# Kernel tuning notes

Measured on AMD Instinct MI355X. Metric: run time of the kernel, lower is better.

The kernel has to match this reference:

```python
import jax, jax.numpy as jnp
import numpy as np

E = 2          # n_modalities
HQ = 16        # n_heads
HK = 8         # n_kv_heads
HD = 128       # head_dim
DIM = 2048
BS = 2
SEQ = 2048
EPS = 1e-6
ROPE_THETA = 10000.0


def _rmsnorm(x, w):
    # x: (..., d), w broadcastable to x
    return x * jax.lax.rsqrt(jnp.mean(x * x, axis=-1, keepdims=True) + EPS) * w


def _apply_rope(t, cos, sin):
    # t: (bs, seq, H, HD); cos/sin: (seq, HD//2). Complex rotation on pairs.
    t2 = t.reshape(*t.shape[:-1], HD // 2, 2)
    t0, t1 = t2[..., 0], t2[..., 1]
    c = cos[None, :, None, :]
    s = sin[None, :, None, :]
    out = jnp.stack([t0 * c - t1 * s, t0 * s + t1 * c], axis=-1)
    return out.reshape(t.shape)


def setup_inputs() -> dict:
    key = jax.random.key(0)
    ks = jax.random.split(key, 8)
    pos = jnp.arange(SEQ, dtype=jnp.float32)
    inv_freq = 1.0 / (ROPE_THETA ** (jnp.arange(0, HD, 2, dtype=jnp.float32) / HD))
    ang = pos[:, None] * inv_freq[None, :]  # (SEQ, HD//2)
    return {
        "x": jax.random.normal(ks[0], (BS, SEQ, DIM), jnp.float32),
        "freqs_cos": jnp.cos(ang),
        "freqs_sin": jnp.sin(ang),
        "wq": jax.random.normal(ks[1], (E, DIM, HQ * HD), jnp.float32) * 0.02,
        "wk": jax.random.normal(ks[2], (E, DIM, HK * HD), jnp.float32) * 0.02,
        "wv": jax.random.normal(ks[3], (E, DIM, HK * HD), jnp.float32) * 0.02,
        "wo": jax.random.normal(ks[4], (E, HQ * HD, DIM), jnp.float32) * 0.02,
        "q_norm_w": jnp.ones((E, HD), jnp.float32),
        "k_norm_w": jnp.ones((E, HD), jnp.float32),
        "attn_norm_w": jnp.ones((E, DIM), jnp.float32),
        "modality_ids": jax.random.randint(ks[5], (BS * SEQ,), 0, E, jnp.int32),
    }


def reference(x, freqs_cos, freqs_sin, wq, wk, wv, wo,
              q_norm_w, k_norm_w, attn_norm_w, modality_ids):
    bs, seq, dim = x.shape
    xf = x.reshape(-1, dim)  # (N, dim)
    onehot = (modality_ids[None, :] == jnp.arange(E, dtype=modality_ids.dtype)[:, None]).astype(x.dtype)  # (E, N)

    # Per-modality QKV projections + QK RMSNorm, then combine by modality id
    q = jnp.einsum('nd,edh->enh', xf, wq).reshape(E, -1, HQ, HD)
    q = _rmsnorm(q, q_norm_w[:, None, None, :])
    q = jnp.einsum('en,enhd->nhd', onehot, q).reshape(bs, seq, HQ, HD)

    k = jnp.einsum('nd,edh->enh', xf, wk).reshape(E, -1, HK, HD)
    k = _rmsnorm(k, k_norm_w[:, None, None, :])
    k = jnp.einsum('en,enhd->nhd', onehot, k).reshape(bs, seq, HK, HD)

    v = jnp.einsum('nd,edh->enh', xf, wv).reshape(E, -1, HK, HD)
    v = jnp.einsum('en,enhd->nhd', onehot, v).reshape(bs, seq, HK, HD)

    # RoPE
    q = _apply_rope(q, freqs_cos, freqs_sin)
    k = _apply_rope(k, freqs_cos, freqs_sin)

    # repeat_kv for GQA
    n_rep = HQ // HK
    k = jnp.repeat(k, n_rep, axis=2)
    v = jnp.repeat(v, n_rep, axis=2)

    # Global causal SDPA
    qh = jnp.swapaxes(q, 1, 2)  # (bs, HQ, seq, HD)
    kh = jnp.swapaxes(k, 1, 2)
    vh = jnp.swapaxes(v, 1, 2)
    scores = jnp.einsum('bhqd,bhkd->bhqk', qh, kh) / jnp.sqrt(jnp.asarray(HD, x.dtype))
    causal = jnp.tril(jnp.ones((seq, seq), dtype=bool))
    scores = jnp.where(causal[None, None], scores, jnp.asarray(-1e30, x.dtype))
    attn = jax.nn.softmax(scores, axis=-1)
    out = jnp.einsum('bhqk,bhkd->bhqd', attn, vh)
    out_flat = jnp.swapaxes(out, 1, 2).reshape(-1, HQ * HD)  # (N, HQ*HD)

    # Per-modality output projection + RMSNorm, combine
    o = jnp.einsum('nh,ehd->end', out_flat, wo)  # (E, N, dim)
    o = _rmsnorm(o, attn_norm_w[:, None, :])
    o = jnp.einsum('en,end->nd', onehot, o)
    return o.reshape(bs, seq, dim)
```

## Files before the change

### kernel.cpp

```cpp
#include <hip/hip_runtime.h>

#define E_ 2
#define HQ_ 16
#define HK_ 8
#define HD_ 128
#define DIM_ 2048
#define BS_ 2
#define SEQ_ 2048
#define NTOK 4096

typedef unsigned short ushort_t;
typedef short bf16x8 __attribute__((ext_vector_type(8)));
typedef unsigned short ushort8 __attribute__((ext_vector_type(8)));
typedef float f32x4 __attribute__((ext_vector_type(4)));

#define MFMA(a, b, c) __builtin_amdgcn_mfma_f32_16x16x32_bf16(a, b, c, 0, 0, 0)

__device__ __forceinline__ unsigned short f2bf(float f) {
  unsigned u = __builtin_bit_cast(unsigned, f);
  u = (u + 0x7FFFu + ((u >> 16) & 1u)) >> 16;
  return (unsigned short)u;
}
__device__ __forceinline__ float bf2f(unsigned short h) {
  unsigned u = ((unsigned)h) << 16;
  return __builtin_bit_cast(float, u);
}

__device__ __forceinline__ void glds16(const void* g, void* s) {
  __builtin_amdgcn_global_load_lds(
      (const __attribute__((address_space(1))) unsigned int*)g,
      (__attribute__((address_space(3))) unsigned int*)s, 16, 0, 0);
}

__global__ __launch_bounds__(1024) void build_crow(const int* __restrict__ ids,
                                                   int* __restrict__ cnt, int* __restrict__ crow) {
  __shared__ int sc[1024];
  __shared__ int total0;
  const int t = threadIdx.x;
  int id4[4];
  int c = 0;
  for (int j = 0; j < 4; j++) {
    id4[j] = ids[t * 4 + j];
    c += (id4[j] == 0);
  }
  sc[t] = c;
  __syncthreads();
  for (int off = 1; off < 1024; off <<= 1) {
    int v = sc[t];
    int add = (t >= off) ? sc[t - off] : 0;
    __syncthreads();
    sc[t] = v + add;
    __syncthreads();
  }
  if (t == 1023) total0 = sc[1023];
  __syncthreads();
  const int cnt0 = total0;
  if (t == 0) {
    cnt[0] = cnt0;
    cnt[1] = NTOK - cnt0;
  }
  int p0 = sc[t] - c;
  int r0 = 0;
  for (int j = 0; j < 4; j++) {
    int n = t * 4 + j;
    int cr;
    if (id4[j] == 0) {
      cr = p0 + r0;
      r0++;
    } else {
      cr = cnt0 + (n - (p0 + r0));
    }
    crow[n] = cr;
  }
}

__global__ __launch_bounds__(256) void convert_scatter(const float* __restrict__ x,
                                                       const int* __restrict__ crow,
                                                       ushort_t* __restrict__ xb) {
  const int token = blockIdx.x;
  const int cr = crow[token];
  const long src = (long)token * DIM_ + threadIdx.x * 8;
  const long dst = (long)cr * DIM_ + threadIdx.x * 8;
  float4 a = *(const float4*)(x + src);
  float4 b = *(const float4*)(x + src + 4);
  ushort8 o;
  o[0] = f2bf(a.x); o[1] = f2bf(a.y); o[2] = f2bf(a.z); o[3] = f2bf(a.w);
  o[4] = f2bf(b.x); o[5] = f2bf(b.y); o[6] = f2bf(b.z); o[7] = f2bf(b.w);
  *(ushort8*)(xb + dst) = o;
}

__global__ __launch_bounds__(256) void transpose_f2b(const float* __restrict__ in,
                                                     ushort_t* __restrict__ out, int K, int N,
                                                     long inE, long outE, int outBase) {
  __shared__ float tile[32][33];
  int e = blockIdx.z;
  const float* inp = in + (long)e * inE;
  ushort_t* outp = out + (long)e * outE;
  int n0 = blockIdx.x * 32, k0 = blockIdx.y * 32;
  int tx = threadIdx.x & 31, ty = threadIdx.x >> 5;
  for (int i = 0; i < 4; i++)
    tile[ty + i * 8][tx] = inp[(long)(k0 + ty + i * 8) * N + n0 + tx];
  __syncthreads();
  for (int i = 0; i < 4; i++)
    outp[(long)(outBase + n0 + ty + i * 8) * K + k0 + tx] = f2bf(tile[tx][ty + i * 8]);
}

__global__ __launch_bounds__(256) void transpose_v(const ushort_t* __restrict__ qkv,
                                                   const int* __restrict__ crow,
                                                   ushort_t* __restrict__ vt) {
  __shared__ ushort_t tile[32][34];
  int z = blockIdx.z;
  int b = z / HK_, hk = z % HK_;
  int s0 = blockIdx.x * 32, d0 = blockIdx.y * 32;
  int tx = threadIdx.x & 31, ty = threadIdx.x >> 5;
  for (int i = 0; i < 4; i++) {
    int cr = crow[b * SEQ_ + s0 + ty + i * 8];
    tile[ty + i * 8][tx] = qkv[(long)cr * 4096 + 3072 + hk * 128 + d0 + tx];
  }
  __syncthreads();
  for (int i = 0; i < 4; i++)
    vt[((long)(b * HK_ + hk) * 128 + d0 + ty + i * 8) * SEQ_ + s0 + tx] = tile[tx][ty + i * 8];
}

__global__ __launch_bounds__(512, 2) void gemm_bt_8ph(const ushort_t* __restrict__ A,
                                                      const ushort_t* __restrict__ BT,
                                                      ushort_t* __restrict__ C, int K, int Nc,
                                                      const int* __restrict__ cnt, long btE) {
  __shared__ __align__(16) char lds[131072];
  const int bm = blockIdx.x, bn = blockIdx.y, e = blockIdx.z;
  const int cnt0 = cnt[0];
  const int scnt = e ? (NTOK - cnt0) : cnt0;
  if (bm * 256 >= scnt) return;
  const int sbase = e ? cnt0 : 0;
  const ushort_t* Bte = BT + (long)e * btE;

  const int t = threadIdx.x, w = t >> 6, lane = t & 63;
  const int quad = lane >> 4, l16 = lane & 15;
  const int wr = w >> 2, wc = w & 3;
  const int nh = wc >> 1;

  const int arow0 = sbase + bm * 256;
  const int brow0 = bn * 256;

  const int srow = t >> 2;
  const int lc = ((t & 3) - (srow >> 1)) & 3;
  int ga0 = arow0 + srow;        if (ga0 > NTOK - 1) ga0 = NTOK - 1;
  int ga1 = arow0 + 128 + srow;  if (ga1 > NTOK - 1) ga1 = NTOK - 1;
  const ushort_t* sA0 = A + (long)ga0 * K + lc * 8;
  const ushort_t* sA1 = A + (long)ga1 * K + lc * 8;
  const ushort_t* sB0 = Bte + (long)(brow0 + srow) * K + lc * 8;
  const ushort_t* sB1 = Bte + (long)(brow0 + 128 + srow) * K + lc * 8;

  char* ldsw = (char*)lds + w * 1024;
  const int aoffF = wr * 16384;
  const int boffF = 32768 + nh * 16384;

  f32x4 acc[8][4];
#pragma unroll
  for (int i = 0; i < 8; i++)
#pragma unroll
    for (int j = 0; j < 4; j++) acc[i][j] = (f32x4){0.f, 0.f, 0.f, 0.f};

  bf16x8 bfr[4];

#define STAGE_A(bufbyte, ks, kk)                                              \
  glds16(sA0 + (kk) + (ks) * 32, ldsw + (bufbyte) + (0 * 2 + (ks)) * 8192);   \
  glds16(sA1 + (kk) + (ks) * 32, ldsw + (bufbyte) + (1 * 2 + (ks)) * 8192);
#define STAGE_B(bufbyte, ks, kk)                                                      \
  glds16(sB0 + (kk) + (ks) * 32, ldsw + (bufbyte) + 32768 + (0 * 2 + (ks)) * 8192);   \
  glds16(sB1 + (kk) + (ks) * 32, ldsw + (bufbyte) + 32768 + (1 * 2 + (ks)) * 8192);

#define PHASE(ks, mfh, LOADB, STG)                                                        \
  {                                                                                       \
    bf16x8 af[4];                                                                         \
    _Pragma("unroll") for (int i = 0; i < 4; i++) {                                       \
      const int r = ((mfh)*4 + i) * 16 + l16;                                             \
      af[i] = *(const bf16x8*)(Ab + (ks)*8192 + r * 64 + ((quad + (r >> 1)) & 3) * 16);   \
    }                                                                                     \
    if (LOADB) {                                                                          \
      _Pragma("unroll") for (int nf = 0; nf < 4; nf++) {                                  \
        const int r = (wc & 1) * 64 + nf * 16 + l16;                                      \
        bfr[nf] = *(const bf16x8*)(Bb + (ks)*8192 + r * 64 + ((quad + (r >> 1)) & 3) * 16); \
      }                                                                                   \
    }                                                                                     \
    STG;                                                                                  \
    __builtin_amdgcn_s_barrier();                                                         \
    asm volatile("s_waitcnt lgkmcnt(0)" ::: "memory");                                    \
    __builtin_amdgcn_sched_barrier(0);                                                    \
    __builtin_amdgcn_s_setprio(1);                                                        \
    _Pragma("unroll") for (int i = 0; i < 4; i++)                                         \
        _Pragma("unroll") for (int nf = 0; nf < 4; nf++)                                  \
            acc[(mfh)*4 + i][nf] = MFMA(af[i], bfr[nf], acc[(mfh)*4 + i][nf]);            \
    __builtin_amdgcn_s_setprio(0);                                                        \
    __builtin_amdgcn_s_barrier();                                                         \
  }

  STAGE_A(0, 0, 0);
  STAGE_B(0, 0, 0);
  STAGE_A(0, 1, 0);
  STAGE_B(0, 1, 0);
  asm volatile("s_waitcnt vmcnt(0)" ::: "memory");
  __builtin_amdgcn_s_barrier();

  const int NT = K >> 6;
  for (int kt = 0; kt < NT; kt++) {
    const int bufb = (kt & 1) << 16;
    const int nxtb = bufb ^ 65536;
    const int k1 = (kt + 1) << 6;
    const bool st = (kt + 1) < NT;
    const char* Ab = (const char*)lds + bufb + aoffF;
    const char* Bb = (const char*)lds + bufb + boffF;

    PHASE(0, 0, 1,
          if (st) { STAGE_A(nxtb, 0, k1); asm volatile("s_waitcnt vmcnt(4)" ::: "memory"); }
          else { asm volatile("s_waitcnt vmcnt(0)" ::: "memory"); })
    PHASE(0, 1, 0,
          if (st) { STAGE_B(nxtb, 0, k1); asm volatile("s_waitcnt vmcnt(4)" ::: "memory"); }
          else { asm volatile("s_waitcnt vmcnt(0)" ::: "memory"); })
    PHASE(1, 0, 1,
          if (st) { STAGE_A(nxtb, 1, k1); asm volatile("s_waitcnt vmcnt(4)" ::: "memory"); }
          else { asm volatile("s_waitcnt vmcnt(0)" ::: "memory"); })
    PHASE(1, 1, 0,
          if (st) { STAGE_B(nxtb, 1, k1); asm volatile("s_waitcnt vmcnt(4)" ::: "memory"); }
          else { asm volatile("s_waitcnt vmcnt(0)" ::: "memory"); })
  }
#undef PHASE
#undef STAGE_A
#undef STAGE_B

#pragma unroll
  for (int mf = 0; mf < 8; mf++) {
#pragma unroll
    for (int reg = 0; reg < 4; reg++) {
      const int rl = wr * 128 + mf * 16 + quad * 4 + reg;
      if (bm * 256 + rl >= scnt) continue;
      ushort_t* Cp = C + (long)(arow0 + rl) * Nc + brow0 + wc * 64 + l16;
#pragma unroll
      for (int nf = 0; nf < 4; nf++) Cp[nf * 16] = f2bf(acc[mf][nf][reg]);
    }
  }
}

__global__ __launch_bounds__(256) void fuse_rmsrope(
    const ushort_t* __restrict__ qkv, const int* __restrict__ crow, const float* __restrict__ qw,
    const float* __restrict__ kw, const float* __restrict__ fc, const float* __restrict__ fs,
    const int* __restrict__ ids, ushort_t* __restrict__ qout, ushort_t* __restrict__ kout) {
  const int token = blockIdx.x;
  const int slot = blockIdx.y * 4 + (threadIdx.x >> 6);
  const int lane = threadIdx.x & 63;
  const int b = token >> 11, s = token & 2047;
  const int e = ids[token];
  const int cr = crow[token];
  const bool isq = slot < 16;
  const int h = isq ? slot : slot - 16;
  const ushort_t* src = qkv + (long)cr * 4096 + (isq ? slot * 128 : 2048 + h * 128);
  unsigned pv = *(const unsigned*)(src + 2 * lane);
  float v0 = bf2f((unsigned short)pv), v1 = bf2f((unsigned short)(pv >> 16));
  float ss = v0 * v0 + v1 * v1;
  ss += __shfl_xor(ss, 32); ss += __shfl_xor(ss, 16); ss += __shfl_xor(ss, 8);
  ss += __shfl_xor(ss, 4);  ss += __shfl_xor(ss, 2);  ss += __shfl_xor(ss, 1);
  float r = rsqrtf(ss * (1.0f / 128.0f) + 1e-6f);
  const float* nw = (isq ? qw : kw) + e * 128;
  v0 *= r * nw[2 * lane];
  v1 *= r * nw[2 * lane + 1];
  float c = fc[s * 64 + lane], sn = fs[s * 64 + lane];
  float o0 = v0 * c - v1 * sn;
  float o1 = v0 * sn + v1 * c;
  ushort_t* dst;
  if (isq) {
    const float QS = 0.08838834764831845f * 1.4426950408889634f;
    o0 *= QS; o1 *= QS;
    dst = qout + ((long)(b * HQ_ + h) * SEQ_ + s) * 128;
  } else {
    dst = kout + ((long)(b * HK_ + h) * SEQ_ + s) * 128;
  }
  *(unsigned*)(dst + 2 * lane) = (unsigned)f2bf(o0) | ((unsigned)f2bf(o1) << 16);
}

__global__ __launch_bounds__(256, 2) void attn_kernel(const ushort_t* __restrict__ Q,
                                                      const ushort_t* __restrict__ K,
                                                      const ushort_t* __restrict__ VT,
                                                      const int* __restrict__ crow,
                                                      ushort_t* __restrict__ O) {
  __shared__ __align__(16) ushort_t Qs[64 * 128];
  __shared__ __align__(16) ushort_t Ks[64 * 128];
  __shared__ __align__(16) ushort_t Vs[128 * 64];
  __shared__ __align__(16) ushort_t Ps[4][16][72];

  const int bh = blockIdx.y;
  const int b = bh >> 4, h = bh & 15, hk = h >> 1;
  const int qi = 31 - blockIdx.x;
  const int q0 = qi * 64;
  const int t = threadIdx.x, w = t >> 6, lane = t & 63;
  const int quad = lane >> 4, l16 = lane & 15;

  const ushort_t* qbase = Q + ((long)(b * HQ_ + h) * SEQ_) * HD_;
  const ushort_t* kbase = K + ((long)(b * HK_ + hk) * SEQ_) * HD_;
  const ushort_t* vtbase = VT + ((long)(b * HK_ + hk) * HD_) * SEQ_;

  for (int c = 0; c < 4; c++) {
    int lin = c * 4096 + w * 1024 + lane * 16;
    int row = lin >> 8;
    int gc = (((lin >> 4) & 15) - row) & 15;
    glds16(qbase + (long)(q0 + row) * HD_ + gc * 8, (char*)Qs + c * 4096 + w * 1024);
  }
  __syncthreads();
  bf16x8 qf[4];
  {
    int row = w * 16 + l16;
    for (int kk = 0; kk < 4; kk++) {
      int cl = (kk * 4 + quad + row) & 15;
      qf[kk] = *(const bf16x8*)((const char*)Qs + row * 256 + cl * 16);
    }
  }

  const f32x4 zero = {0.f, 0.f, 0.f, 0.f};
  f32x4 oa[8];
  for (int i = 0; i < 8; i++) oa[i] = zero;
  float rs[4] = {0.f, 0.f, 0.f, 0.f};

  const int nkt = qi + 1;
  for (int kt = 0; kt < nkt; kt++) {
    const int s0 = kt * 64;
    for (int c = 0; c < 4; c++) {
      int lin = c * 4096 + w * 1024 + lane * 16;
      int row = lin >> 8;
      int gc = (((lin >> 4) & 15) - row) & 15;
      glds16(kbase + (long)(s0 + row) * HD_ + gc * 8, (char*)Ks + c * 4096 + w * 1024);
      int d = lin >> 7;
      int gc2 = (((lin >> 4) & 7) - d) & 7;
      glds16(vtbase + (long)d * SEQ_ + s0 + gc2 * 8, (char*)Vs + c * 4096 + w * 1024);
    }
    __syncthreads();

    f32x4 sa[4];
    for (int cb = 0; cb < 4; cb++) {
      sa[cb] = zero;
      int n = cb * 16 + l16;
      for (int kk = 0; kk < 4; kk++) {
        int cl = (kk * 4 + quad + n) & 15;
        bf16x8 kfrag = *(const bf16x8*)((const char*)Ks + n * 256 + cl * 16);
        sa[cb] = MFMA(qf[kk], kfrag, sa[cb]);
      }
    }
    if (kt == nkt - 1) {
      for (int cb = 0; cb < 4; cb++)
        for (int r = 0; r < 4; r++)
          if (cb * 16 + l16 > q0 + w * 16 + quad * 4 + r - s0) sa[cb][r] = -1e30f;
    }
    for (int cb = 0; cb < 4; cb++)
      for (int r = 0; r < 4; r++) {
        float p = exp2f(sa[cb][r]);
        rs[r] += p;
        Ps[w][quad * 4 + r][cb * 16 + l16] = f2bf(p);
      }
    for (int kk2 = 0; kk2 < 2; kk2++) {
      bf16x8 pf = *(const bf16x8*)&Ps[w][l16][kk2 * 32 + quad * 8];
      for (int vb = 0; vb < 8; vb++) {
        int d = vb * 16 + l16;
        int cl = (kk2 * 4 + quad + d) & 7;
        bf16x8 vfrag = *(const bf16x8*)((const char*)Vs + d * 128 + cl * 16);
        oa[vb] = MFMA(pf, vfrag, oa[vb]);
      }
    }
    __syncthreads();
  }
  float inv[4];
  int cr4[4];
  for (int r = 0; r < 4; r++) {
    float v = rs[r];
    v += __shfl_xor(v, 1);
    v += __shfl_xor(v, 2);
    v += __shfl_xor(v, 4);
    v += __shfl_xor(v, 8);
    inv[r] = 1.0f / v;
    cr4[r] = crow[b * SEQ_ + q0 + w * 16 + quad * 4 + r];
  }
  for (int vb = 0; vb < 8; vb++)
    for (int r = 0; r < 4; r++) {
      long off = (long)cr4[r] * 2048 + h * 128 + vb * 16 + l16;
      O[off] = f2bf(oa[vb][r] * inv[r]);
    }
}

__global__ __launch_bounds__(256) void out_rmsnorm(const ushort_t* __restrict__ o_raw,
                                                   const int* __restrict__ crow,
                                                   const float* __restrict__ wn,
                                                   const int* __restrict__ ids,
                                                   float* __restrict__ out) {
  __shared__ float red[4];
  const int token = blockIdx.x;
  const int t = threadIdx.x, w = t >> 6, lane = t & 63;
  const int e = ids[token];
  const int cr = crow[token];
  ushort8 u = *(const ushort8*)(o_raw + (long)cr * 2048 + t * 8);
  float v[8];
  float ss = 0.f;
  for (int j = 0; j < 8; j++) {
    v[j] = bf2f(u[j]);
    ss += v[j] * v[j];
  }
  ss += __shfl_xor(ss, 32); ss += __shfl_xor(ss, 16); ss += __shfl_xor(ss, 8);
  ss += __shfl_xor(ss, 4);  ss += __shfl_xor(ss, 2);  ss += __shfl_xor(ss, 1);
  if (lane == 0) red[w] = ss;
  __syncthreads();
  float tot = red[0] + red[1] + red[2] + red[3];
  float r = rsqrtf(tot * (1.0f / 2048.0f) + 1e-6f);
  const float* wp = wn + (long)e * 2048 + t * 8;
  float* op = out + (long)token * 2048 + t * 8;
  for (int j = 0; j < 8; j++) op[j] = v[j] * r * wp[j];
}

extern "C" void kernel_launch(void* const* d_in, const int* in_sizes, int n_in, void* d_out,
                              int out_size, void* d_ws, size_t ws_size, hipStream_t stream) {
  const float* x = (const float*)d_in[0];
  const float* fc = (const float*)d_in[1];
  const float* fs = (const float*)d_in[2];
  const float* wq = (const float*)d_in[3];
  const float* wk = (const float*)d_in[4];
  const float* wv = (const float*)d_in[5];
  const float* wo = (const float*)d_in[6];
  const float* qnw = (const float*)d_in[7];
  const float* knw = (const float*)d_in[8];
  const float* anw = (const float*)d_in[9];
  const int* ids = (const int*)d_in[10];
  float* out = (float*)d_out;
  char* ws = (char*)d_ws;

  ushort_t* x_bf = (ushort_t*)(ws + 0);
  ushort_t* wqkvT = (ushort_t*)(ws + (16l << 20));
  ushort_t* woT = (ushort_t*)(ws + (16l << 20));
  int* cnt = (int*)(ws + (48l << 20));
  int* crow = (int*)(ws + (48l << 20) + 64);
  ushort_t* qkvraw = (ushort_t*)(ws + (64l << 20));
  ushort_t* qfh = (ushort_t*)(ws + (96l << 20));
  ushort_t* kfh = (ushort_t*)(ws + (112l << 20));
  ushort_t* vt = (ushort_t*)(ws + (120l << 20));
  ushort_t* o_flat = x_bf;
  ushort_t* o_raw = qkvraw;

  build_crow<<<1, 1024, 0, stream>>>(ids, cnt, crow);
  convert_scatter<<<NTOK, 256, 0, stream>>>(x, crow, x_bf);
  transpose_f2b<<<dim3(64, 64, E_), 256, 0, stream>>>(wq, wqkvT, 2048, 2048, (long)2048 * 2048,
                                                      (long)4096 * 2048, 0);
  transpose_f2b<<<dim3(32, 64, E_), 256, 0, stream>>>(wk, wqkvT, 2048, 1024, (long)2048 * 1024,
                                                      (long)4096 * 2048, 2048);
  transpose_f2b<<<dim3(32, 64, E_), 256, 0, stream>>>(wv, wqkvT, 2048, 1024, (long)2048 * 1024,
                                                      (long)4096 * 2048, 3072);
  gemm_bt_8ph<<<dim3(16, 16, E_), 512, 0, stream>>>(x_bf, wqkvT, qkvraw, 2048, 4096, cnt,
                                                    (long)4096 * 2048);
  transpose_f2b<<<dim3(64, 64, E_), 256, 0, stream>>>(wo, woT, 2048, 2048, (long)2048 * 2048,
                                                      (long)2048 * 2048, 0);
  fuse_rmsrope<<<dim3(NTOK, 6), 256, 0, stream>>>(qkvraw, crow, qnw, knw, fc, fs, ids, qfh, kfh);
  transpose_v<<<dim3(64, 4, BS_ * HK_), 256, 0, stream>>>(qkvraw, crow, vt);
  attn_kernel<<<dim3(32, 32), 256, 0, stream>>>(qfh, kfh, vt, crow, o_flat);
  gemm_bt_8ph<<<dim3(16, 8, E_), 512, 0, stream>>>(o_flat, woT, o_raw, 2048, 2048, cnt,
                                                   (long)2048 * 2048);
  out_rmsnorm<<<NTOK, 256, 0, stream>>>(o_raw, crow, anw, ids, out);
}
```

Before: 517.1 us.

## Pair causal query tiles per block and double-buffer K/V tiles in attention

Each attention block now handles two query tiles, qi and 31-qi, so every block does the same amount of causal work, and the grid is halved. K/V tiles are double-buffered in shared memory: the next tile is prefetched while the current one is computed, and Q is staged through the first K buffer. This removes load imbalance across causal tiles and hides global-to-LDS latency. The cost is twice the K/V shared memory, which may reduce occupancy, and fewer blocks in flight.

```diff
diff --git a/kernel.cpp b/kernel.cpp
--- a/kernel.cpp
+++ b/kernel.cpp
@@ -282,15 +282,12 @@
                                                       const ushort_t* __restrict__ VT,
                                                       const int* __restrict__ crow,
                                                       ushort_t* __restrict__ O) {
-  __shared__ __align__(16) ushort_t Qs[64 * 128];
-  __shared__ __align__(16) ushort_t Ks[64 * 128];
-  __shared__ __align__(16) ushort_t Vs[128 * 64];
+  __shared__ __align__(16) ushort_t Ks[2][64 * 128];
+  __shared__ __align__(16) ushort_t Vs[2][128 * 64];
   __shared__ __align__(16) ushort_t Ps[4][16][72];
 
   const int bh = blockIdx.y;
   const int b = bh >> 4, h = bh & 15, hk = h >> 1;
-  const int qi = 31 - blockIdx.x;
-  const int q0 = qi * 64;
   const int t = threadIdx.x, w = t >> 6, lane = t & 63;
   const int quad = lane >> 4, l16 = lane & 15;
 
@@ -298,89 +295,106 @@
   const ushort_t* kbase = K + ((long)(b * HK_ + hk) * SEQ_) * HD_;
   const ushort_t* vtbase = VT + ((long)(b * HK_ + hk) * HD_) * SEQ_;
 
-  for (int c = 0; c < 4; c++) {
-    int lin = c * 4096 + w * 1024 + lane * 16;
-    int row = lin >> 8;
-    int gc = (((lin >> 4) & 15) - row) & 15;
-    glds16(qbase + (long)(q0 + row) * HD_ + gc * 8, (char*)Qs + c * 4096 + w * 1024);
-  }
-  __syncthreads();
-  bf16x8 qf[4];
-  {
-    int row = w * 16 + l16;
-    for (int kk = 0; kk < 4; kk++) {
-      int cl = (kk * 4 + quad + row) & 15;
-      qf[kk] = *(const bf16x8*)((const char*)Qs + row * 256 + cl * 16);
-    }
+#define STAGEKV(bi, s0)                                                                     \
+  for (int c = 0; c < 4; c++) {                                                             \
+    int lin = c * 4096 + w * 1024 + lane * 16;                                              \
+    int row = lin >> 8;                                                                     \
+    int gc = (((lin >> 4) & 15) - row) & 15;                                                \
+    glds16(kbase + (long)((s0) + row) * HD_ + gc * 8, (char*)Ks[bi] + c * 4096 + w * 1024); \
+    int d = lin >> 7;                                                                       \
+    int gc2 = (((lin >> 4) & 7) - d) & 7;                                                   \
+    glds16(vtbase + (long)d * SEQ_ + (s0) + gc2 * 8, (char*)Vs[bi] + c * 4096 + w * 1024);  \
   }
 
   const f32x4 zero = {0.f, 0.f, 0.f, 0.f};
-  f32x4 oa[8];
-  for (int i = 0; i < 8; i++) oa[i] = zero;
-  float rs[4] = {0.f, 0.f, 0.f, 0.f};
-
-  const int nkt = qi + 1;
-  for (int kt = 0; kt < nkt; kt++) {
-    const int s0 = kt * 64;
+
+  for (int half = 0; half < 2; half++) {
+    const int qi = half ? (int)blockIdx.x : 31 - (int)blockIdx.x;
+    const int q0 = qi * 64;
+
     for (int c = 0; c < 4; c++) {
       int lin = c * 4096 + w * 1024 + lane * 16;
       int row = lin >> 8;
       int gc = (((lin >> 4) & 15) - row) & 15;
-      glds16(kbase + (long)(s0 + row) * HD_ + gc * 8, (char*)Ks + c * 4096 + w * 1024);
-      int d = lin >> 7;
-      int gc2 = (((lin >> 4) & 7) - d) & 7;
-      glds16(vtbase + (long)d * SEQ_ + s0 + gc2 * 8, (char*)Vs + c * 4096 + w * 1024);
+      glds16(qbase + (long)(q0 + row) * HD_ + gc * 8, (char*)Ks[0] + c * 4096 + w * 1024);
     }
     __syncthreads();
-
-    f32x4 sa[4];
-    for (int cb = 0; cb < 4; cb++) {
-      sa[cb] = zero;
-      int n = cb * 16 + l16;
+    bf16x8 qf[4];
+    {
+      int row = w * 16 + l16;
       for (int kk = 0; kk < 4; kk++) {
-        int cl = (kk * 4 + quad + n) & 15;
-        bf16x8 kfrag = *(const bf16x8*)((const char*)Ks + n * 256 + cl * 16);
-        sa[cb] = MFMA(qf[kk], kfrag, sa[cb]);
+        int cl = (kk * 4 + quad + row) & 15;
+        qf[kk] = *(const bf16x8*)((const char*)Ks[0] + row * 256 + cl * 16);
       }
     }
-    if (kt == nkt - 1) {
+    __syncthreads();
+
+    f32x4 oa[8];
+    for (int i = 0; i < 8; i++) oa[i] = zero;
+    float rs[4] = {0.f, 0.f, 0.f, 0.f};
+
+    const int nkt = qi + 1;
+    STAGEKV(0, 0);
+    __syncthreads();
+    int buf = 0;
+    for (int kt = 0; kt < nkt; kt++) {
+      const int s0 = kt * 64;
+      if (kt + 1 < nkt) STAGEKV(buf ^ 1, s0 + 64);
+      const char* Kb = (const char*)Ks[buf];
+      const char* Vb = (const char*)Vs[buf];
+
+      f32x4 sa[4];
+      for (int cb = 0; cb < 4; cb++) {
+        sa[cb] = zero;
+        int n = cb * 16 + l16;
+        for (int kk = 0; kk < 4; kk++) {
+          int cl = (kk * 4 + quad + n) & 15;
+          bf16x8 kfrag = *(const bf16x8*)(Kb + n * 256 + cl * 16);
+          sa[cb] = MFMA(qf[kk], kfrag, sa[cb]);
+        }
+      }
+      if (kt == nkt - 1) {
+        for (int cb = 0; cb < 4; cb++)
+          for (int r = 0; r < 4; r++)
+            if (cb * 16 + l16 > q0 + w * 16 + quad * 4 + r - s0) sa[cb][r] = -1e30f;
+      }
       for (int cb = 0; cb < 4; cb++)
-        for (int r = 0; r < 4; r++)
-          if (cb * 16 + l16 > q0 + w * 16 + quad * 4 + r - s0) sa[cb][r] = -1e30f;
-    }
-    for (int cb = 0; cb < 4; cb++)
+        for (int r = 0; r < 4; r++) {
+          float p = exp2f(sa[cb][r]);
+          rs[r] += p;
+          Ps[w][quad * 4 + r][cb * 16 + l16] = f2bf(p);
+        }
+      for (int kk2 = 0; kk2 < 2; kk2++) {
+        bf16x8 pf = *(const bf16x8*)&Ps[w][l16][kk2 * 32 + quad * 8];
+        for (int vb = 0; vb < 8; vb++) {
+          int d = vb * 16 + l16;
+          int cl = (kk2 * 4 + quad + d) & 7;
+          bf16x8 vfrag = *(const bf16x8*)(Vb + d * 128 + cl * 16);
+          oa[vb] = MFMA(pf, vfrag, oa[vb]);
+        }
+      }
+      __syncthreads();
+      buf ^= 1;
+    }
+
+    float inv[4];
+    int cr4[4];
+    for (int r = 0; r < 4; r++) {
+      float v = rs[r];
+      v += __shfl_xor(v, 1);
+      v += __shfl_xor(v, 2);
+      v += __shfl_xor(v, 4);
+      v += __shfl_xor(v, 8);
+      inv[r] = 1.0f / v;
+      cr4[r] = crow[b * SEQ_ + q0 + w * 16 + quad * 4 + r];
+    }
+    for (int vb = 0; vb < 8; vb++)
       for (int r = 0; r < 4; r++) {
-        float p = exp2f(sa[cb][r]);
-        rs[r] += p;
-        Ps[w][quad * 4 + r][cb * 16 + l16] = f2bf(p);
+        long off = (long)cr4[r] * 2048 + h * 128 + vb * 16 + l16;
+        O[off] = f2bf(oa[vb][r] * inv[r]);
       }
-    for (int kk2 = 0; kk2 < 2; kk2++) {
-      bf16x8 pf = *(const bf16x8*)&Ps[w][l16][kk2 * 32 + quad * 8];
-      for (int vb = 0; vb < 8; vb++) {
-        int d = vb * 16 + l16;
-        int cl = (kk2 * 4 + quad + d) & 7;
-        bf16x8 vfrag = *(const bf16x8*)((const char*)Vs + d * 128 + cl * 16);
-        oa[vb] = MFMA(pf, vfrag, oa[vb]);
-      }
-    }
-    __syncthreads();
-  }
-  float inv[4];
-  int cr4[4];
-  for (int r = 0; r < 4; r++) {
-    float v = rs[r];
-    v += __shfl_xor(v, 1);
-    v += __shfl_xor(v, 2);
-    v += __shfl_xor(v, 4);
-    v += __shfl_xor(v, 8);
-    inv[r] = 1.0f / v;
-    cr4[r] = crow[b * SEQ_ + q0 + w * 16 + quad * 4 + r];
-  }
-  for (int vb = 0; vb < 8; vb++)
-    for (int r = 0; r < 4; r++) {
-      long off = (long)cr4[r] * 2048 + h * 128 + vb * 16 + l16;
-      O[off] = f2bf(oa[vb][r] * inv[r]);
-    }
+  }
+#undef STAGEKV
 }
 
 __global__ __launch_bounds__(256) void out_rmsnorm(const ushort_t* __restrict__ o_raw,
@@ -453,7 +467,7 @@
                                                       (long)2048 * 2048, 0);
   fuse_rmsrope<<<dim3(NTOK, 6), 256, 0, stream>>>(qkvraw, crow, qnw, knw, fc, fs, ids, qfh, kfh);
   transpose_v<<<dim3(64, 4, BS_ * HK_), 256, 0, stream>>>(qkvraw, crow, vt);
-  attn_kernel<<<dim3(32, 32), 256, 0, stream>>>(qfh, kfh, vt, crow, o_flat);
+  attn_kernel<<<dim3(16, 32), 256, 0, stream>>>(qfh, kfh, vt, crow, o_flat);
   gemm_bt_8ph<<<dim3(16, 8, E_), 512, 0, stream>>>(o_flat, woT, o_raw, 2048, 2048, cnt,
                                                    (long)2048 * 2048);
   out_rmsnorm<<<NTOK, 256, 0, stream>>>(o_raw, crow, anw, ids, out);
```

After: 462.9 us. 1.12x faster.
